# Performance work log

Hardware: AMD Instinct MI355X
Metric: run time of the kernel (lower is better)

## Reference

```python
import jax, jax.numpy as jnp
import numpy as np

DIM = 768
NUM_HEAD = 12
DIM_HEAD = DIM // NUM_HEAD
SCALE = DIM_HEAD ** -0.5
B, N = 4, 1024


def setup_inputs() -> dict:
    key = jax.random.key(0)
    ks = jax.random.split(key, 6)
    return {
        "x": jax.random.normal(ks[0], (B, N, DIM), jnp.float32),
        "q_weight": jax.random.normal(ks[1], (DIM, DIM), jnp.float32) * 0.02,
        "k_weight": jax.random.normal(ks[2], (DIM, DIM), jnp.float32) * 0.02,
        "v_weight": jax.random.normal(ks[3], (DIM, DIM), jnp.float32) * 0.02,
        "q_bias": jnp.zeros((DIM,), jnp.float32),
        "k_bias": jnp.zeros((DIM,), jnp.float32),
        "v_bias": jnp.zeros((DIM,), jnp.float32),
        "proj_weight": jax.random.normal(ks[4], (DIM, DIM), jnp.float32) * 0.02,
        "proj_bias": jax.random.normal(ks[5], (DIM,), jnp.float32) * 0.02,
    }


def reference(x, q_weight, k_weight, v_weight, q_bias, k_bias, v_bias,
              proj_weight, proj_bias):
    B_, N_, C = x.shape
    shortcut = x
    # pre-norm: torch .std() is unbiased (ddof=1)
    mean = jnp.mean(x, axis=-1, keepdims=True)
    std = jnp.std(x, axis=-1, keepdims=True, ddof=1)
    xn = (x - mean) / std
    # F.linear: x @ W.T + b
    q = xn @ q_weight.T + q_bias
    k = xn @ k_weight.T + k_bias
    v = xn @ v_weight.T + v_bias
    # b n (h d) -> b h n d
    q = q.reshape(B_, N_, NUM_HEAD, DIM_HEAD).transpose(0, 2, 1, 3)
    k = k.reshape(B_, N_, NUM_HEAD, DIM_HEAD).transpose(0, 2, 1, 3)
    v = v.reshape(B_, N_, NUM_HEAD, DIM_HEAD).transpose(0, 2, 1, 3)
    attn = jnp.einsum('bhqd,bhkd->bhqk', q, k * SCALE)
    attn = jax.nn.softmax(attn, axis=-1)
    out = jnp.einsum('bhqk,bhkd->bhqd', attn, v)
    out = out.transpose(0, 2, 1, 3).reshape(B_, N_, C)
    out = out @ proj_weight.T + proj_bias
    return out + shortcut
```

## Files before the change

kernel.cpp:

```cpp
#include <hip/hip_runtime.h>

typedef unsigned short ushort_t;
typedef unsigned int uint_t;
typedef __attribute__((ext_vector_type(8))) unsigned short ushort8;
typedef __attribute__((ext_vector_type(2))) unsigned int uint2v;
typedef __attribute__((ext_vector_type(8))) __bf16 bf16x8;
typedef __attribute__((ext_vector_type(4))) float floatx4;

#define DIM 768
#define NHEAD 12
#define DHEAD 64
#define SEQ 1024
#define BATCH 4
#define TOKENS (BATCH * SEQ)
#define WELEM (DIM * DIM)
#define SCALE_LOG2E 0.18033688011112042f

static __device__ __forceinline__ uint_t fbits(float f) {
  union { float f; uint_t u; } c; c.f = f; return c.u;
}
static __device__ __forceinline__ ushort_t f2bf(float f) {
  return (ushort_t)((fbits(f) + 0x8000u) >> 16);
}
static __device__ __forceinline__ uint_t pack_bf2(float lo, float hi) {
  const uint_t a = fbits(lo) + 0x8000u, b = fbits(hi) + 0x8000u;
#if __has_builtin(__builtin_amdgcn_perm)
  return __builtin_amdgcn_perm(b, a, 0x07060302u);
#else
  return (a >> 16) | (b & 0xFFFF0000u);
#endif
}
static __device__ __forceinline__ float fexp2(float x) {
#if __has_builtin(__builtin_amdgcn_exp2f)
  return __builtin_amdgcn_exp2f(x);
#else
  return exp2f(x);
#endif
}
static __device__ __forceinline__ floatx4 mfma16(ushort8 a, ushort8 b, floatx4 c) {
  return __builtin_amdgcn_mfma_f32_16x16x32_bf16(
      __builtin_bit_cast(bf16x8, a), __builtin_bit_cast(bf16x8, b), c, 0, 0, 0);
}
static __device__ __forceinline__ void gload_lds16(const ushort_t* g,
                                                   ushort_t* l) {
  __builtin_amdgcn_global_load_lds(
      (const __attribute__((address_space(1))) void*)g,
      (__attribute__((address_space(3))) void*)l, 16, 0, 0);
}

__global__ __launch_bounds__(256) void prep_kernel(
    const float* __restrict__ qw, const float* __restrict__ kw,
    const float* __restrict__ vw, const float* __restrict__ pw,
    const float* __restrict__ x, ushort_t* __restrict__ wbf,
    ushort_t* __restrict__ xn) {
  const int bid = blockIdx.x;
  if (bid < 2304) {
    const int mat = bid / 576, inner = bid % 576;
    const float* s = (mat == 0) ? qw : (mat == 1) ? kw : (mat == 2) ? vw : pw;
    ushort_t* d = wbf + (size_t)mat * WELEM;
    const int i = (inner * 256 + threadIdx.x) * 4;
    const float4 f = *(const float4*)&s[i];
    uint2v o;
    o[0] = pack_bf2(f.x, f.y);
    o[1] = pack_bf2(f.z, f.w);
    *(uint2v*)&d[i] = o;
  } else {
    const int wave = threadIdx.x >> 6, lane = threadIdx.x & 63;
    const int row = (bid - 2304) * 4 + wave;
    const float4* xr = (const float4*)(x + (size_t)row * DIM);
    float4 v[3];
    float s = 0.f, s2 = 0.f;
#pragma unroll
    for (int j = 0; j < 3; ++j) {
      v[j] = xr[j * 64 + lane];
      s += v[j].x + v[j].y + v[j].z + v[j].w;
      s2 += v[j].x * v[j].x + v[j].y * v[j].y + v[j].z * v[j].z +
            v[j].w * v[j].w;
    }
#pragma unroll
    for (int off = 1; off < 64; off <<= 1) {
      s += __shfl_xor(s, off);
      s2 += __shfl_xor(s2, off);
    }
    const float mean = s * (1.f / 768.f);
    const float var = (s2 - 768.f * mean * mean) * (1.f / 767.f);
    const float rstd = rsqrtf(var);
    ushort_t* xo = xn + (size_t)row * DIM;
#pragma unroll
    for (int j = 0; j < 3; ++j) {
      uint2v o;
      o[0] = pack_bf2((v[j].x - mean) * rstd, (v[j].y - mean) * rstd);
      o[1] = pack_bf2((v[j].z - mean) * rstd, (v[j].w - mean) * rstd);
      *(uint2v*)&xo[(j * 64 + lane) * 4] = o;
    }
  }
}

#define BK 64
#define NKIT (DIM / BK)
__global__ __launch_bounds__(256) void qkv_kernel(
    const ushort_t* __restrict__ xn, const ushort_t* __restrict__ wbf,
    const float* __restrict__ qb, const float* __restrict__ kb,
    const float* __restrict__ vb,
    ushort_t* __restrict__ qh, ushort_t* __restrict__ kh,
    ushort_t* __restrict__ vt) {
  __shared__ ushort_t As[2][128 * BK];
  __shared__ ushort_t Bs[2][128 * BK];
  const int tid = threadIdx.x;
  const int wave = tid >> 6, lane = tid & 63, quad = lane >> 4, l15 = lane & 15;
  const int m0 = blockIdx.x * 128;
  const int mat = blockIdx.y / 6, nb = blockIdx.y % 6;
  const int n0 = nb * 128;
  const ushort_t* W = wbf + (size_t)mat * WELEM;
  const int chan_off = (wave >> 1) * 64, tok_off = (wave & 1) * 64;
  const int srow8 = lane >> 3;
  const int schunk = (lane & 7) ^ srow8;
  const int l7 = l15 & 7;

  floatx4 acc[4][4];
#pragma unroll
  for (int i = 0; i < 4; ++i)
#pragma unroll
    for (int j = 0; j < 4; ++j) acc[i][j] = (floatx4){0.f, 0.f, 0.f, 0.f};

  auto stage = [&](int k0, int bf) {
#pragma unroll
    for (int i = 0; i < 4; ++i) {
      const int c = wave * 4 + i;
      const int row = c * 8 + srow8;
      gload_lds16(&xn[(size_t)(m0 + row) * DIM + k0 + schunk * 8],
                  &As[bf][c * 512]);
      gload_lds16(&W[(size_t)(n0 + row) * DIM + k0 + schunk * 8],
                  &Bs[bf][c * 512]);
    }
  };

  stage(0, 0);
  for (int it = 0; it < NKIT; ++it) {
    const int cur = it & 1;
    __syncthreads();
    if (it + 1 < NKIT) stage((it + 1) * BK, cur ^ 1);
    ushort8 af[4][2], bfr[4][2];
#pragma unroll
    for (int i = 0; i < 4; ++i)
#pragma unroll
      for (int k2 = 0; k2 < 2; ++k2) {
        const int ch = ((k2 * 4 + quad) ^ l7) * 8;
        bfr[i][k2] = *(const ushort8*)&Bs[cur][(chan_off + i * 16 + l15) * BK + ch];
        af[i][k2] = *(const ushort8*)&As[cur][(tok_off + i * 16 + l15) * BK + ch];
      }
#pragma unroll
    for (int k2 = 0; k2 < 2; ++k2)
#pragma unroll
      for (int i = 0; i < 4; ++i)
#pragma unroll
        for (int j = 0; j < 4; ++j)
          acc[i][j] = mfma16(bfr[i][k2], af[j][k2], acc[i][j]);
  }

  if (mat != 2) {
    const float* bias = (mat == 0) ? qb : kb;
    ushort_t* dst = (mat == 0) ? qh : kh;
    const float os = (mat == 0) ? SCALE_LOG2E : 1.0f;
    const int hh = (n0 + chan_off) >> 6;
#pragma unroll
    for (int i = 0; i < 4; ++i) {
      const int ch0 = n0 + chan_off + i * 16 + quad * 4;
      const float4 bv = *(const float4*)&bias[ch0];
      const int d0 = i * 16 + quad * 4;
#pragma unroll
      for (int j = 0; j < 4; ++j) {
        const int tok = m0 + tok_off + j * 16 + l15;
        const int bb = tok >> 10, nn = tok & 1023;
        uint2v pk;
        pk[0] = pack_bf2((acc[i][j][0] + bv.x) * os, (acc[i][j][1] + bv.y) * os);
        pk[1] = pack_bf2((acc[i][j][2] + bv.z) * os, (acc[i][j][3] + bv.w) * os);
        *(uint2v*)&dst[(size_t)((bb * NHEAD + hh) * SEQ + nn) * DHEAD + d0] = pk;
      }
    }
  } else {
#pragma unroll
    for (int i = 0; i < 4; ++i) {
      const int ch0 = n0 + chan_off + i * 16 + quad * 4;
      const float4 bv = *(const float4*)&vb[ch0];
      const float bvf[4] = {bv.x, bv.y, bv.z, bv.w};
      const int hh = ch0 >> 6, d0 = ch0 & 63;
#pragma unroll
      for (int j = 0; j < 4; ++j) {
        const int tok = m0 + tok_off + j * 16 + l15;
        const int bb = tok >> 10, nn = tok & 1023;
        const int t2 = (nn >> 4) & 3;
        const int goff = (nn & ~63) + l15 * 4 + t2;
        const size_t base = (size_t)((bb * NHEAD + hh) * DHEAD + d0) * SEQ;
#pragma unroll
        for (int r = 0; r < 4; ++r)
          vt[base + (size_t)r * SEQ + goff] = f2bf(acc[i][j][r] + bvf[r]);
      }
    }
  }
}

#define PSTR 68
__global__ __launch_bounds__(256) void attn_kernel(
    const ushort_t* __restrict__ qh, const ushort_t* __restrict__ kh,
    const ushort_t* __restrict__ vt, ushort_t* __restrict__ ao) {
  __shared__ ushort_t kv[2][2][4096];
  __shared__ ushort_t Ps[4][16 * PSTR];
  float* cb = (float*)&kv[0][0][0];
  const int tid = threadIdx.x;
  const int wave = tid >> 6, lane = tid & 63, quad = lane >> 4, l15 = lane & 15;
  const int l7 = l15 & 7;
  const int grp = wave >> 1, wsub = wave & 1;
  const int h = blockIdx.y, b = blockIdx.z;
  const int basekv = ((b * NHEAD + h) * SEQ) * DHEAD;
  const int basevt = ((b * NHEAD + h) * DHEAD) * SEQ;
  const int q0 = blockIdx.x * 64 + wsub * 32;
  const int kbase = grp * 512;

  ushort8 qf[2][2];
#pragma unroll
  for (int w = 0; w < 2; ++w) {
    const ushort_t* Qr = qh + basekv + (q0 + w * 16 + l15) * DHEAD;
    qf[w][0] = *(const ushort8*)&Qr[quad * 8];
    qf[w][1] = *(const ushort8*)&Qr[32 + quad * 8];
  }
  ushort8 ones;
#pragma unroll
  for (int i = 0; i < 8; ++i) ones[i] = 0x3F80;

  floatx4 o[2][4];
#pragma unroll
  for (int w = 0; w < 2; ++w)
#pragma unroll
    for (int t = 0; t < 4; ++t) o[w][t] = (floatx4){0.f, 0.f, 0.f, 0.f};
  floatx4 acc_l[2] = {(floatx4){0.f, 0.f, 0.f, 0.f},
                      (floatx4){0.f, 0.f, 0.f, 0.f}};

  const int srow8 = lane >> 3, schunk = (lane & 7) ^ srow8;

  for (int kt = 0; kt < 512; kt += 64) {
#pragma unroll
    for (int i = 0; i < 4; ++i) {
      const int c = wsub * 4 + i;
      gload_lds16(&kh[basekv + (kbase + kt + c * 8 + srow8) * DHEAD + schunk * 8],
                  &kv[grp][0][c * 512]);
      gload_lds16(&vt[basevt + (c * 8 + srow8) * SEQ + kbase + kt + schunk * 8],
                  &kv[grp][1][c * 512]);
    }
    __syncthreads();

    floatx4 sacc[2][4];
#pragma unroll
    for (int w = 0; w < 2; ++w)
#pragma unroll
      for (int s = 0; s < 4; ++s) sacc[w][s] = (floatx4){0.f, 0.f, 0.f, 0.f};
#pragma unroll
    for (int s = 0; s < 4; ++s) {
#pragma unroll
      for (int hh = 0; hh < 2; ++hh) {
        const ushort8 kf = *(const ushort8*)&kv[grp][0][(s * 16 + l15) * 64 +
                                                        (((hh * 4 + quad) ^ l7) * 8)];
#pragma unroll
        for (int w = 0; w < 2; ++w)
          sacc[w][s] = mfma16(qf[w][hh], kf, sacc[w][s]);
      }
    }

#pragma unroll
    for (int w = 0; w < 2; ++w) {
#pragma unroll
      for (int r = 0; r < 4; ++r) {
        uint2v pk;
        pk[0] = pack_bf2(fexp2(sacc[w][0][r]), fexp2(sacc[w][1][r]));
        pk[1] = pack_bf2(fexp2(sacc[w][2][r]), fexp2(sacc[w][3][r]));
        *(uint2v*)&Ps[wave][(quad * 4 + r) * PSTR + l15 * 4] = pk;
      }
    }

#pragma unroll
    for (int hh = 0; hh < 2; ++hh) {
      ushort8 pf[2];
#pragma unroll
      for (int w = 0; w < 2; ++w) {
        pf[w] = *(const ushort8*)&Ps[wave][l15 * PSTR + hh * 32 + quad * 8];
        acc_l[w] = mfma16(pf[w], ones, acc_l[w]);
      }
#pragma unroll
      for (int t = 0; t < 4; ++t) {
        const ushort8 vf = *(const ushort8*)&kv[grp][1][(t * 16 + l15) * 64 +
                                                        (((hh * 4 + quad) ^ l7) * 8)];
#pragma unroll
        for (int w = 0; w < 2; ++w) o[w][t] = mfma16(pf[w], vf, o[w][t]);
      }
    }
    __syncthreads();
  }

  const int cb0 = wsub * (32 * 66);
  if (grp == 1) {
#pragma unroll
    for (int w = 0; w < 2; ++w) {
#pragma unroll
      for (int t = 0; t < 4; ++t)
#pragma unroll
        for (int r = 0; r < 4; ++r)
          cb[cb0 + (w * 16 + quad * 4 + r) * 66 + t * 16 + l15] = o[w][t][r];
      if (l15 == 0)
#pragma unroll
        for (int r = 0; r < 4; ++r)
          cb[cb0 + (w * 16 + quad * 4 + r) * 66 + 64] = acc_l[w][r];
    }
  }
  __syncthreads();
  if (grp == 0) {
#pragma unroll
    for (int w = 0; w < 2; ++w) {
#pragma unroll
      for (int r = 0; r < 4; ++r) {
        const int row = w * 16 + quad * 4 + r;
        const float l = acc_l[w][r] + cb[cb0 + row * 66 + 64];
        const float rl = 1.f / l;
        const int token = b * SEQ + q0 + row;
#pragma unroll
        for (int t = 0; t < 4; ++t) {
          const float val = o[w][t][r] + cb[cb0 + row * 66 + t * 16 + l15];
          ao[(size_t)token * DIM + h * DHEAD + t * 16 + l15] = f2bf(val * rl);
        }
      }
    }
  }
}

__global__ __launch_bounds__(256) void proj_kernel(
    const ushort_t* __restrict__ ao, const ushort_t* __restrict__ pwb,
    const float* __restrict__ pb, const float* __restrict__ x,
    float* __restrict__ out) {
  __shared__ ushort_t As[2][64 * BK];
  __shared__ ushort_t Bs[2][128 * BK];
  const int tid = threadIdx.x;
  const int wave = tid >> 6, lane = tid & 63, quad = lane >> 4, l15 = lane & 15;
  const int m0 = blockIdx.x * 64;
  const int n0 = blockIdx.y * 128;
  const int chan_off = (wave >> 1) * 64, tok_off = (wave & 1) * 32;
  const int srow8 = lane >> 3;
  const int schunk = (lane & 7) ^ srow8;
  const int l7 = l15 & 7;

  floatx4 acc[4][2];
#pragma unroll
  for (int i = 0; i < 4; ++i)
#pragma unroll
    for (int j = 0; j < 2; ++j) acc[i][j] = (floatx4){0.f, 0.f, 0.f, 0.f};

  auto stage = [&](int k0, int bf) {
#pragma unroll
    for (int i = 0; i < 2; ++i) {
      const int c = wave * 2 + i;
      const int row = c * 8 + srow8;
      gload_lds16(&ao[(size_t)(m0 + row) * DIM + k0 + schunk * 8],
                  &As[bf][c * 512]);
    }
#pragma unroll
    for (int i = 0; i < 4; ++i) {
      const int c = wave * 4 + i;
      const int row = c * 8 + srow8;
      gload_lds16(&pwb[(size_t)(n0 + row) * DIM + k0 + schunk * 8],
                  &Bs[bf][c * 512]);
    }
  };

  stage(0, 0);
  for (int it = 0; it < NKIT; ++it) {
    const int cur = it & 1;
    __syncthreads();
    if (it + 1 < NKIT) stage((it + 1) * BK, cur ^ 1);
    ushort8 af[2][2], bfr[4][2];
#pragma unroll
    for (int k2 = 0; k2 < 2; ++k2) {
      const int ch = ((k2 * 4 + quad) ^ l7) * 8;
#pragma unroll
      for (int j = 0; j < 2; ++j)
        af[j][k2] = *(const ushort8*)&As[cur][(tok_off + j * 16 + l15) * BK + ch];
#pragma unroll
      for (int i = 0; i < 4; ++i)
        bfr[i][k2] = *(const ushort8*)&Bs[cur][(chan_off + i * 16 + l15) * BK + ch];
    }
#pragma unroll
    for (int k2 = 0; k2 < 2; ++k2)
#pragma unroll
      for (int i = 0; i < 4; ++i)
#pragma unroll
        for (int j = 0; j < 2; ++j)
          acc[i][j] = mfma16(bfr[i][k2], af[j][k2], acc[i][j]);
  }

#pragma unroll
  for (int i = 0; i < 4; ++i) {
    const int ch0 = n0 + chan_off + i * 16 + quad * 4;
    const float4 bv = *(const float4*)&pb[ch0];
#pragma unroll
    for (int j = 0; j < 2; ++j) {
      const int tok = m0 + tok_off + j * 16 + l15;
      const float4 res = *(const float4*)&x[(size_t)tok * DIM + ch0];
      float4 ov;
      ov.x = acc[i][j][0] + bv.x + res.x;
      ov.y = acc[i][j][1] + bv.y + res.y;
      ov.z = acc[i][j][2] + bv.z + res.z;
      ov.w = acc[i][j][3] + bv.w + res.w;
      *(float4*)&out[(size_t)tok * DIM + ch0] = ov;
    }
  }
}

extern "C" void kernel_launch(void* const* d_in, const int* in_sizes, int n_in,
                              void* d_out, int out_size, void* d_ws,
                              size_t ws_size, hipStream_t stream) {
  const float* x  = (const float*)d_in[0];
  const float* qw = (const float*)d_in[1];
  const float* kw = (const float*)d_in[2];
  const float* vw = (const float*)d_in[3];
  const float* qb = (const float*)d_in[4];
  const float* kb = (const float*)d_in[5];
  const float* vb = (const float*)d_in[6];
  const float* pw = (const float*)d_in[7];
  const float* pb = (const float*)d_in[8];
  float* out = (float*)d_out;

  ushort_t* ws = (ushort_t*)d_ws;
  const size_t NTOK = (size_t)TOKENS * DIM;
  ushort_t* xn  = ws;
  ushort_t* qh  = ws + NTOK;
  ushort_t* kh  = ws + 2 * NTOK;
  ushort_t* vt  = ws + 3 * NTOK;
  ushort_t* wbf = ws + 4 * NTOK;
  ushort_t* ao  = xn;

  prep_kernel<<<2304 + TOKENS / 4, 256, 0, stream>>>(qw, kw, vw, pw, x, wbf, xn);
  qkv_kernel<<<dim3(32, 18), 256, 0, stream>>>(xn, wbf, qb, kb, vb, qh, kh, vt);
  attn_kernel<<<dim3(16, NHEAD, BATCH), 256, 0, stream>>>(qh, kh, vt, ao);
  proj_kernel<<<dim3(64, 6), 256, 0, stream>>>(ao, wbf + 3 * (size_t)WELEM, pb,
                                               x, out);
}
```

Before: 156.8 us.

## Load GEMM activation fragments directly from global memory, shrink QKV token tile

In both the QKV and projection GEMMs, the activation operand is no longer staged through LDS. Each lane now reads its MFMA fragments straight from global memory, while the weights stay double-buffered in LDS. The QKV kernel's token tile is halved to 64, which doubles the grid. This removes the LDS traffic and footprint for activations and raises occupancy, but global loads now sit on the critical path without prefetch, and different waves re-read the same activation rows.

```diff
diff --git a/kernel.cpp b/kernel.cpp
--- a/kernel.cpp
+++ b/kernel.cpp
@@ -104,33 +104,34 @@
     const float* __restrict__ vb,
     ushort_t* __restrict__ qh, ushort_t* __restrict__ kh,
     ushort_t* __restrict__ vt) {
-  __shared__ ushort_t As[2][128 * BK];
   __shared__ ushort_t Bs[2][128 * BK];
   const int tid = threadIdx.x;
   const int wave = tid >> 6, lane = tid & 63, quad = lane >> 4, l15 = lane & 15;
-  const int m0 = blockIdx.x * 128;
+  const int m0 = blockIdx.x * 64;
   const int mat = blockIdx.y / 6, nb = blockIdx.y % 6;
   const int n0 = nb * 128;
   const ushort_t* W = wbf + (size_t)mat * WELEM;
-  const int chan_off = (wave >> 1) * 64, tok_off = (wave & 1) * 64;
+  const int chan_off = (wave >> 1) * 64, tok_off = (wave & 1) * 32;
   const int srow8 = lane >> 3;
   const int schunk = (lane & 7) ^ srow8;
   const int l7 = l15 & 7;
 
-  floatx4 acc[4][4];
+  floatx4 acc[4][2];
 #pragma unroll
   for (int i = 0; i < 4; ++i)
 #pragma unroll
-    for (int j = 0; j < 4; ++j) acc[i][j] = (floatx4){0.f, 0.f, 0.f, 0.f};
+    for (int j = 0; j < 2; ++j) acc[i][j] = (floatx4){0.f, 0.f, 0.f, 0.f};
+
+  const ushort_t* arow[2];
+#pragma unroll
+  for (int j = 0; j < 2; ++j)
+    arow[j] = &xn[(size_t)(m0 + tok_off + j * 16 + l15) * DIM];
 
   auto stage = [&](int k0, int bf) {
 #pragma unroll
     for (int i = 0; i < 4; ++i) {
       const int c = wave * 4 + i;
-      const int row = c * 8 + srow8;
-      gload_lds16(&xn[(size_t)(m0 + row) * DIM + k0 + schunk * 8],
-                  &As[bf][c * 512]);
-      gload_lds16(&W[(size_t)(n0 + row) * DIM + k0 + schunk * 8],
+      gload_lds16(&W[(size_t)(n0 + c * 8 + srow8) * DIM + k0 + schunk * 8],
                   &Bs[bf][c * 512]);
     }
   };
@@ -138,23 +139,28 @@
   stage(0, 0);
   for (int it = 0; it < NKIT; ++it) {
     const int cur = it & 1;
+    const int k0 = it * BK;
     __syncthreads();
-    if (it + 1 < NKIT) stage((it + 1) * BK, cur ^ 1);
-    ushort8 af[4][2], bfr[4][2];
+    if (it + 1 < NKIT) stage(k0 + BK, cur ^ 1);
+    ushort8 af[2][2];
+#pragma unroll
+    for (int j = 0; j < 2; ++j)
+#pragma unroll
+      for (int k2 = 0; k2 < 2; ++k2)
+        af[j][k2] = *(const ushort8*)&arow[j][k0 + (k2 * 4 + quad) * 8];
+    ushort8 bfr[4][2];
 #pragma unroll
     for (int i = 0; i < 4; ++i)
 #pragma unroll
-      for (int k2 = 0; k2 < 2; ++k2) {
-        const int ch = ((k2 * 4 + quad) ^ l7) * 8;
-        bfr[i][k2] = *(const ushort8*)&Bs[cur][(chan_off + i * 16 + l15) * BK + ch];
-        af[i][k2] = *(const ushort8*)&As[cur][(tok_off + i * 16 + l15) * BK + ch];
-      }
+      for (int k2 = 0; k2 < 2; ++k2)
+        bfr[i][k2] = *(const ushort8*)&Bs[cur][(chan_off + i * 16 + l15) * BK +
+                                              (((k2 * 4 + quad) ^ l7) * 8)];
 #pragma unroll
     for (int k2 = 0; k2 < 2; ++k2)
 #pragma unroll
       for (int i = 0; i < 4; ++i)
 #pragma unroll
-        for (int j = 0; j < 4; ++j)
+        for (int j = 0; j < 2; ++j)
           acc[i][j] = mfma16(bfr[i][k2], af[j][k2], acc[i][j]);
   }
 
@@ -169,7 +175,7 @@
       const float4 bv = *(const float4*)&bias[ch0];
       const int d0 = i * 16 + quad * 4;
 #pragma unroll
-      for (int j = 0; j < 4; ++j) {
+      for (int j = 0; j < 2; ++j) {
         const int tok = m0 + tok_off + j * 16 + l15;
         const int bb = tok >> 10, nn = tok & 1023;
         uint2v pk;
@@ -186,7 +192,7 @@
       const float bvf[4] = {bv.x, bv.y, bv.z, bv.w};
       const int hh = ch0 >> 6, d0 = ch0 & 63;
 #pragma unroll
-      for (int j = 0; j < 4; ++j) {
+      for (int j = 0; j < 2; ++j) {
         const int tok = m0 + tok_off + j * 16 + l15;
         const int bb = tok >> 10, nn = tok & 1023;
         const int t2 = (nn >> 4) & 3;
@@ -335,7 +341,6 @@
     const ushort_t* __restrict__ ao, const ushort_t* __restrict__ pwb,
     const float* __restrict__ pb, const float* __restrict__ x,
     float* __restrict__ out) {
-  __shared__ ushort_t As[2][64 * BK];
   __shared__ ushort_t Bs[2][128 * BK];
   const int tid = threadIdx.x;
   const int wave = tid >> 6, lane = tid & 63, quad = lane >> 4, l15 = lane & 15;
@@ -352,19 +357,16 @@
 #pragma unroll
     for (int j = 0; j < 2; ++j) acc[i][j] = (floatx4){0.f, 0.f, 0.f, 0.f};
 
+  const ushort_t* arow[2];
+#pragma unroll
+  for (int j = 0; j < 2; ++j)
+    arow[j] = &ao[(size_t)(m0 + tok_off + j * 16 + l15) * DIM];
+
   auto stage = [&](int k0, int bf) {
-#pragma unroll
-    for (int i = 0; i < 2; ++i) {
-      const int c = wave * 2 + i;
-      const int row = c * 8 + srow8;
-      gload_lds16(&ao[(size_t)(m0 + row) * DIM + k0 + schunk * 8],
-                  &As[bf][c * 512]);
-    }
 #pragma unroll
     for (int i = 0; i < 4; ++i) {
       const int c = wave * 4 + i;
-      const int row = c * 8 + srow8;
-      gload_lds16(&pwb[(size_t)(n0 + row) * DIM + k0 + schunk * 8],
+      gload_lds16(&pwb[(size_t)(n0 + c * 8 + srow8) * DIM + k0 + schunk * 8],
                   &Bs[bf][c * 512]);
     }
   };
@@ -372,19 +374,22 @@
   stage(0, 0);
   for (int it = 0; it < NKIT; ++it) {
     const int cur = it & 1;
+    const int k0 = it * BK;
     __syncthreads();
-    if (it + 1 < NKIT) stage((it + 1) * BK, cur ^ 1);
-    ushort8 af[2][2], bfr[4][2];
-#pragma unroll
-    for (int k2 = 0; k2 < 2; ++k2) {
-      const int ch = ((k2 * 4 + quad) ^ l7) * 8;
-#pragma unroll
-      for (int j = 0; j < 2; ++j)
-        af[j][k2] = *(const ushort8*)&As[cur][(tok_off + j * 16 + l15) * BK + ch];
-#pragma unroll
-      for (int i = 0; i < 4; ++i)
-        bfr[i][k2] = *(const ushort8*)&Bs[cur][(chan_off + i * 16 + l15) * BK + ch];
-    }
+    if (it + 1 < NKIT) stage(k0 + BK, cur ^ 1);
+    ushort8 af[2][2];
+#pragma unroll
+    for (int j = 0; j < 2; ++j)
+#pragma unroll
+      for (int k2 = 0; k2 < 2; ++k2)
+        af[j][k2] = *(const ushort8*)&arow[j][k0 + (k2 * 4 + quad) * 8];
+    ushort8 bfr[4][2];
+#pragma unroll
+    for (int i = 0; i < 4; ++i)
+#pragma unroll
+      for (int k2 = 0; k2 < 2; ++k2)
+        bfr[i][k2] = *(const ushort8*)&Bs[cur][(chan_off + i * 16 + l15) * BK +
+                                              (((k2 * 4 + quad) ^ l7) * 8)];
 #pragma unroll
     for (int k2 = 0; k2 < 2; ++k2)
 #pragma unroll
@@ -436,7 +441,7 @@
   ushort_t* ao  = xn;
 
   prep_kernel<<<2304 + TOKENS / 4, 256, 0, stream>>>(qw, kw, vw, pw, x, wbf, xn);
-  qkv_kernel<<<dim3(32, 18), 256, 0, stream>>>(xn, wbf, qb, kb, vb, qh, kh, vt);
+  qkv_kernel<<<dim3(64, 18), 256, 0, stream>>>(xn, wbf, qb, kb, vb, qh, kh, vt);
   attn_kernel<<<dim3(16, NHEAD, BATCH), 256, 0, stream>>>(qh, kh, vt, ao);
   proj_kernel<<<dim3(64, 6), 256, 0, stream>>>(ao, wbf + 3 * (size_t)WELEM, pb,
                                                x, out);
```

Result: slower. 169.3 us (+8.0%).
